# Kernel optimization log

Measured on AMD Instinct MI355X. Metric: run time of the kernel, lower is better.

## Reference

```python
import jax, jax.numpy as jnp
import numpy as np

DT = 0.05

def _conv(x, w):
    # x: [N,C,H,W], w: [O,I,kh,kw], SAME padding
    return jax.lax.conv_general_dilated(x, w, (1, 1), 'SAME',
                                        dimension_numbers=('NCHW', 'OIHW', 'NCHW'))

def _gru(h, x, wx, wh):
    # convolutional GRU cell (used for Bayesian jumps and SpatialGRU)
    xr, xz, xg = jnp.split(_conv(x, wx), 3, axis=1)
    hr, hz, hg = jnp.split(_conv(h, wh), 3, axis=1)
    r = jax.nn.sigmoid(xr + hr)
    z = jax.nn.sigmoid(xz + hz)
    g = jnp.tanh(xg + r * hg)
    return (1.0 - z) * h + z * g

def _ode_step(h, wrz, wg, dt):
    # GRU-ODE cell, explicit Euler: dh/dt = (1-z)*(g-h)
    r, z = jnp.split(jax.nn.sigmoid(_conv(h, wrz)), 2, axis=1)
    g = jnp.tanh(_conv(r * h, wg))
    return h + dt * (1.0 - z) * (g - h)

def _sgru(x, h0, wx, wh):
    # SpatialGRU: conv-GRU recurrence over the sequence dim
    def step(h, xt):
        h = _gru(h, xt, wx, wh)
        return h, h
    _, hs = jax.lax.scan(step, h0, x.transpose(1, 0, 2, 3, 4))
    return hs.transpose(1, 0, 2, 3, 4)

def setup_inputs() -> dict:
    key = jax.random.key(0)
    B, C, H, W = 2, 64, 64, 64
    Nc, Nl, NF = 3, 5, 6
    ks = jax.random.split(key, 16)
    f = lambda i, s: jax.random.normal(ks[i], s, jnp.float32)
    w = lambda i, s: 0.05 * jax.random.normal(ks[i], s, jnp.float32)
    inp = {}
    inp['future_prediction_input'] = f(0, (B, C, H, W))
    inp['camera_states'] = f(1, (B, Nc, C, H, W))
    inp['lidar_states'] = f(2, (B, Nl, C, H, W))
    # ragged obs times as exact multiples of DT; targets after all obs
    inp['camera_timestamp'] = jnp.broadcast_to(jnp.array([0., 2., 4.]) * DT, (B, Nc)).astype(jnp.float32)
    inp['lidar_timestamp'] = jnp.broadcast_to(jnp.array([1., 3., 5., 6., 7.]) * DT, (B, Nl)).astype(jnp.float32)
    inp['target_timestamp'] = jnp.broadcast_to(jnp.arange(8., 14.) * DT, (B, NF)).astype(jnp.float32)
    inp['ode_wrz'] = w(3, (2 * C, C, 3, 3))
    inp['ode_wg'] = w(4, (C, C, 3, 3))
    inp['jmp_wx'] = w(5, (3 * C, C, 3, 3))
    inp['jmp_wh'] = w(6, (3 * C, C, 3, 3))
    inp['sg0_wx'] = w(7, (3 * C, C, 3, 3))
    inp['sg0_wh'] = w(8, (3 * C, C, 3, 3))
    inp['sg1_wx'] = w(9, (3 * C, C, 3, 3))
    inp['sg1_wh'] = w(10, (3 * C, C, 3, 3))
    inp['res0_w1'] = w(11, (C, C, 3, 3))
    inp['res0_w2'] = w(12, (C, C, 3, 3))
    inp['dl_w1'] = w(13, (128, C, 3, 3))
    inp['dl_w2'] = w(14, (C, 128, 1, 1))
    return inp

def reference(future_prediction_input, camera_states, lidar_states,
              camera_timestamp, lidar_timestamp, target_timestamp,
              ode_wrz, ode_wg, jmp_wx, jmp_wh,
              sg0_wx, sg0_wh, sg1_wx, sg1_wh,
              res0_w1, res0_w2, dl_w1, dl_w2):
    dt = DT
    B, C, H, W = future_prediction_input.shape
    Nc, Nl, NF = camera_timestamp.shape[1], lidar_timestamp.shape[1], target_timestamp.shape[1]
    n_steps = Nc + Nl + NF  # static Euler grid covering all obs + target times
    # --- batched ragged merge: scatter obs onto the time grid (replaces per-sample dict sort) ---
    all_t = jnp.concatenate([camera_timestamp, lidar_timestamp], axis=1)          # [B, Nc+Nl]
    all_obs = jnp.concatenate([camera_states, lidar_states], axis=1)              # [B, Nc+Nl, C, H, W]
    steps = jnp.round(all_t / dt).astype(jnp.int32)
    bidx = jnp.arange(B)[:, None]
    grid = jnp.zeros((B, n_steps, C, H, W), all_obs.dtype).at[bidx, steps].set(all_obs)
    mask = jnp.zeros((B, n_steps), jnp.float32).at[bidx, steps].set(1.0)
    # --- ODE-RNN with Bayesian jumps: jump at obs, Euler-evolve between ---
    def ode_scan(h, xs):
        obs_t, m = xs
        hj = _gru(h, obs_t, jmp_wx, jmp_wh)
        h = jnp.where(m[:, None, None, None] > 0, hj, h)
        h = _ode_step(h, ode_wrz, ode_wg, dt)
        return h, h
    _, hs = jax.lax.scan(ode_scan, future_prediction_input,
                         (grid.transpose(1, 0, 2, 3, 4), mask.T))
    tsteps = jnp.round(target_timestamp / dt).astype(jnp.int32) - 1               # state after step k is time (k+1)*dt
    x = hs.transpose(1, 0, 2, 3, 4)[bidx, tsteps]                                 # [B, NF, C, H, W]
    auxilary_loss = jnp.float32(0.0)
    # --- spatial GRU stack + res blocks / DeepLab head ---
    hidden = x[:, 0]
    x = _sgru(x, hidden, sg0_wx, sg0_wh)
    xf = x.reshape(B * NF, C, H, W)
    xf = xf + _conv(jax.nn.relu(_conv(xf, res0_w1)), res0_w2)                     # residual Block
    x = xf.reshape(B, NF, C, H, W)
    x = _sgru(x, hidden, sg1_wx, sg1_wh)
    xf = x.reshape(B * NF, C, H, W)
    xf = _conv(jax.nn.relu(_conv(xf, dl_w1)), dl_w2)                              # DeepLabHead (3x3 -> relu -> 1x1)
    x = xf.reshape(B, NF, C, H, W)
    return (x, auxilary_loss)
```

## Files before the change

### kernel.cpp

```cpp
#include <hip/hip_runtime.h>
#include <stdint.h>

#define HWP 4096
#define SB  262144LL
#define FB  1572864LL
#define SLABU 1572864LL
#define DTC 0.05f

typedef short short4v __attribute__((ext_vector_type(4)));
typedef short short8v __attribute__((ext_vector_type(8)));
typedef float f32x16  __attribute__((ext_vector_type(16)));

__device__ __forceinline__ float sigm(float x) { return 1.f / (1.f + __expf(-x)); }
__device__ __forceinline__ float tanhf_(float x) {
  float a = fabsf(x);
  float t = __expf(-2.f * a);
  float r = (1.f - t) / (1.f + t);
  return x < 0.f ? -r : r;
}
__device__ __forceinline__ float gru1(float h, float xr, float hr, float xz,
                                      float hz, float xg, float hg) {
  float r = sigm(xr + hr);
  float z = sigm(xz + hz);
  float g = tanhf_(xg + r * hg);
  return (1.f - z) * h + z * g;
}
__device__ __forceinline__ float b2f(unsigned int u) {
  return __uint_as_float(u << 16);
}
__device__ __forceinline__ unsigned short f2b(float f) {
  unsigned int x = __float_as_uint(f);
  unsigned int r = (x + 0x7fffu + ((x >> 16) & 1u)) >> 16;
  return (unsigned short)r;
}

struct WJobs {
  const float* src[11];
  unsigned short* dst[11];
  int oc[11];
  int blk_off[12];
};

__global__ __launch_bounds__(256) void convert_all(WJobs jobs)
{
  int b = blockIdx.x;
  int j = 0;
  while (b >= jobs.blk_off[j + 1]) ++j;
  int g = (b - jobs.blk_off[j]) * 256 + threadIdx.x;
  if (g >= jobs.oc[j] * 64) return;
  const float* w = jobs.src[j];
  unsigned short* dst = jobs.dst[j];
  int oc = g >> 6, ic = g & 63;
  int ocg = oc >> 5, m = oc & 31;
  int kh = ic >> 4, ks = (ic >> 3) & 1, jj = ic & 7;
  int lane = m + 32 * ks;
#pragma unroll
  for (int t = 0; t < 9; ++t) {
    float v = w[(size_t)(oc * 64 + ic) * 9 + t];
    unsigned short hi = f2b(v);
    unsigned short lo = f2b(v - b2f(hi));
    size_t fb = ((size_t)(ocg * 4 + kh) * 9 + t) * 1024;
    dst[fb + (size_t)lane * 8 + jj] = hi;
    dst[fb + 512 + (size_t)lane * 8 + jj] = lo;
  }
}

__global__ __launch_bounds__(256) void convert_1x1(
    const float* __restrict__ w, unsigned short* __restrict__ dst)
{
  int g = blockIdx.x * 256 + threadIdx.x;
  if (g >= 64 * 128) return;
  int oc = g >> 7, ic = g & 127;
  int ocg = oc >> 5, m = oc & 31;
  int k = ic >> 4, ksub = (ic >> 3) & 1, j = ic & 7;
  int lane = m + 32 * ksub;
  float v = w[(size_t)oc * 128 + ic];
  unsigned short hi = f2b(v);
  unsigned short lo = f2b(v - b2f(hi));
  size_t fb = (size_t)(ocg * 8 + k) * 1024;
  dst[fb + (size_t)lane * 8 + j] = hi;
  dst[fb + 512 + (size_t)lane * 8 + j] = lo;
}

template<int NR>
__device__ __forceinline__ void stage_rows(
    unsigned short (*lds)[2][66][68], int slot0,
    const float* __restrict__ in_img, int gy0, int tid)
{
  int px = tid & 63, icq = tid >> 6;
  int ic0 = icq * 16;
  float v[NR][16];
#pragma unroll
  for (int r = 0; r < NR; ++r) {
    int gy = gy0 + r;
    if (gy >= 0 && gy < 64) {
#pragma unroll
      for (int i = 0; i < 16; ++i)
        v[r][i] = in_img[(size_t)(ic0 + i) * HWP + (size_t)gy * 64 + px];
    } else {
#pragma unroll
      for (int i = 0; i < 16; ++i) v[r][i] = 0.f;
    }
  }
#pragma unroll
  for (int r = 0; r < NR; ++r) {
    unsigned short hi[16], lo[16];
#pragma unroll
    for (int i = 0; i < 16; ++i) {
      hi[i] = f2b(v[r][i]);
      lo[i] = f2b(v[r][i] - b2f(hi[i]));
    }
    unsigned short* dhi = &lds[slot0 + r][0][px + 1][ic0];
    unsigned short* dlo = &lds[slot0 + r][1][px + 1][ic0];
#pragma unroll
    for (int q = 0; q < 4; ++q) {
      uint2 ph, pl;
      ph.x = (unsigned)hi[q*4+0] | ((unsigned)hi[q*4+1] << 16);
      ph.y = (unsigned)hi[q*4+2] | ((unsigned)hi[q*4+3] << 16);
      pl.x = (unsigned)lo[q*4+0] | ((unsigned)lo[q*4+1] << 16);
      pl.y = (unsigned)lo[q*4+2] | ((unsigned)lo[q*4+3] << 16);
      *(uint2*)&dhi[q*4] = ph;
      *(uint2*)&dlo[q*4] = pl;
    }
  }
}

#define LOAD_B_SLOT(SLOT, kx)                                                 \
  {                                                                           \
    const unsigned short* bph = &lds[SLOT][0][x0 + n + kx][khb];              \
    const unsigned short* bpl = &lds[SLOT][1][x0 + n + kx][khb];              \
    bhi.lo = *(const short4v*)bph; bhi.hi = *(const short4v*)(bph + 4);       \
    blo.lo = *(const short4v*)bpl; blo.hi = *(const short4v*)(bpl + 4);       \
  }

#define MFMA3(CACC, AHI, ALO)                                                 \
  CACC = __builtin_amdgcn_mfma_f32_32x32x16_bf16(AHI, bhi, CACC, 0, 0, 0);    \
  CACC = __builtin_amdgcn_mfma_f32_32x32x16_bf16(ALO, bhi, CACC, 0, 0, 0);    \
  CACC = __builtin_amdgcn_mfma_f32_32x32x16_bf16(AHI, blo, CACC, 0, 0, 0);

__global__ __launch_bounds__(256) void gru_mfma(
    const float* __restrict__ hprev, long long h_is,
    const unsigned short* __restrict__ wfrag,
    const unsigned short* __restrict__ xcs,
    float* __restrict__ hout, long long o_is)
{
  __shared__ __align__(16) unsigned short lds[3][2][66][68];
  int bid = blockIdx.x;
  int img = bid >> 6, y = bid & 63;
  int tid = threadIdx.x;
  int wv = tid >> 6, lane = tid & 63;
  int wchg = wv >> 1, wpx = wv & 1;
  int x0 = wpx * 32;
  int n = lane & 31, ksub = lane >> 5;

  const float* in_img = hprev + (size_t)img * h_is;
  for (int i = tid; i < 3366; i += 256)
    ((uint4*)lds)[i] = make_uint4(0u, 0u, 0u, 0u);
  __syncthreads();
  stage_rows<3>(lds, 0, in_img, y - 1, tid);
  __syncthreads();

  f32x16 cr, cz, cg;
#pragma unroll
  for (int i = 0; i < 16; ++i) { cr[i] = 0.f; cz[i] = 0.f; cg[i] = 0.f; }

#pragma unroll
  for (int kh = 0; kh < 4; ++kh) {
    int khb = kh * 16 + ksub * 8;
#pragma unroll
    for (int kidx = 0; kidx < 9; ++kidx) {
      int ky = kidx / 3, kx = kidx - ky * 3;
      short8v bhi, blo;
      LOAD_B_SLOT(ky, kx);
      const unsigned short* apr =
          wfrag + (((size_t)wchg * 4 + kh) * 9 + kidx) * 1024 + (size_t)lane * 8;
      const unsigned short* apz = apr + (size_t)2 * 4 * 9 * 1024;
      const unsigned short* apg = apr + (size_t)4 * 4 * 9 * 1024;
      short8v arh = *(const short8v*)apr;
      short8v arl = *(const short8v*)(apr + 512);
      short8v azh = *(const short8v*)apz;
      short8v azl = *(const short8v*)(apz + 512);
      short8v agh = *(const short8v*)apg;
      short8v agl = *(const short8v*)(apg + 512);
      MFMA3(cr, arh, arl);
      MFMA3(cz, azh, azl);
      MFMA3(cg, agh, agl);
    }
  }

  const unsigned short* xcb = xcs + (size_t)img * 786432;
#pragma unroll
  for (int reg = 0; reg < 16; ++reg) {
    int crow = (reg & 3) + 8 * (reg >> 2) + 4 * ksub;
    int c = wchg * 32 + crow;
    size_t px = (size_t)y * 64 + x0 + n;
    float xr = b2f(xcb[(size_t)c * HWP + px]);
    float xz = b2f(xcb[(size_t)(c + 64) * HWP + px]);
    float xg = b2f(xcb[(size_t)(c + 128) * HWP + px]);
    float hv = b2f(lds[1][0][x0 + n + 1][c]) + b2f(lds[1][1][x0 + n + 1][c]);
    hout[(size_t)img * o_is + (size_t)c * HWP + px] =
        gru1(hv, xr, cr[reg], xz, cz[reg], xg, cg[reg]);
  }
}

__global__ __launch_bounds__(256) void rzodeg_mfma(
    const float* __restrict__ hsrc,
    const unsigned short* __restrict__ wrzf,
    const unsigned short* __restrict__ wgf,
    float* __restrict__ hdst,
    float* __restrict__ fr, float* __restrict__ hid)
{
  __shared__ __align__(16) unsigned short lds[5][2][66][68];
  int bid = blockIdx.x;
  int img = bid >> 6, y = bid & 63;
  int tid = threadIdx.x;
  int wv = tid >> 6, lane = tid & 63;
  int wchg = wv >> 1, wpx = wv & 1;
  int x0 = wpx * 32;
  int n = lane & 31, ksub = lane >> 5;

  for (int i = tid; i < 5 * 4 * 16; i += 256) {
    int row = i >> 4, q = i & 15;
    int slot = row >> 2, rem = row & 3;
    int plane = rem >> 1;
    int col = (rem & 1) ? 65 : 0;
    ((uint2*)&lds[slot][plane][col][0])[q] = make_uint2(0u, 0u);
  }
  const float* in_img = hsrc + (size_t)img * SB;
  stage_rows<5>(lds, 0, in_img, y - 2, tid);
  __syncthreads();

  f32x16 cr0, cr1, cr2, cz;
#pragma unroll
  for (int i = 0; i < 16; ++i) { cr0[i]=0.f; cr1[i]=0.f; cr2[i]=0.f; cz[i]=0.f; }

#pragma unroll
  for (int kh = 0; kh < 4; ++kh) {
    int khb = kh * 16 + ksub * 8;
#pragma unroll
    for (int kidx = 0; kidx < 9; ++kidx) {
      int ky = kidx / 3, kx = kidx - ky * 3;
      const unsigned short* apr =
          wrzf + (((size_t)wchg * 4 + kh) * 9 + kidx) * 1024 + (size_t)lane * 8;
      const unsigned short* apz = apr + (size_t)2 * 4 * 9 * 1024;
      short8v arh = *(const short8v*)apr;
      short8v arl = *(const short8v*)(apr + 512);
      short8v azh = *(const short8v*)apz;
      short8v azl = *(const short8v*)(apz + 512);
      { short8v bhi, blo; LOAD_B_SLOT(ky, kx);     MFMA3(cr0, arh, arl); }
      { short8v bhi, blo; LOAD_B_SLOT(ky + 1, kx); MFMA3(cr1, arh, arl);
                                                   MFMA3(cz,  azh, azl); }
      { short8v bhi, blo; LOAD_B_SLOT(ky + 2, kx); MFMA3(cr2, arh, arl); }
    }
  }

  float rv0[16], rv1[16], rv2[16], hk[16];
  {
    int pc = x0 + n + 1;
#pragma unroll
    for (int reg = 0; reg < 16; ++reg) {
      int crow = (reg & 3) + 8 * (reg >> 2) + 4 * ksub;
      int c = wchg * 32 + crow;
      float h0 = b2f(lds[1][0][pc][c]) + b2f(lds[1][1][pc][c]);
      float h1 = b2f(lds[2][0][pc][c]) + b2f(lds[2][1][pc][c]);
      float h2 = b2f(lds[3][0][pc][c]) + b2f(lds[3][1][pc][c]);
      rv0[reg] = sigm(cr0[reg]) * h0;
      rv1[reg] = sigm(cr1[reg]) * h1;
      rv2[reg] = sigm(cr2[reg]) * h2;
      hk[reg] = h1;
    }
  }
  __syncthreads();

  {
    int pc = x0 + n + 1;
#pragma unroll
    for (int reg = 0; reg < 16; ++reg) {
      int crow = (reg & 3) + 8 * (reg >> 2) + 4 * ksub;
      int c = wchg * 32 + crow;
      unsigned short h0 = f2b(rv0[reg]), l0 = f2b(rv0[reg] - b2f(h0));
      unsigned short h1 = f2b(rv1[reg]), l1 = f2b(rv1[reg] - b2f(h1));
      unsigned short h2 = f2b(rv2[reg]), l2 = f2b(rv2[reg] - b2f(h2));
      lds[0][0][pc][c] = h0; lds[0][1][pc][c] = l0;
      lds[1][0][pc][c] = h1; lds[1][1][pc][c] = l1;
      lds[2][0][pc][c] = h2; lds[2][1][pc][c] = l2;
    }
  }
  __syncthreads();

  f32x16 cg;
#pragma unroll
  for (int i = 0; i < 16; ++i) cg[i] = 0.f;
#pragma unroll
  for (int kh = 0; kh < 4; ++kh) {
    int khb = kh * 16 + ksub * 8;
#pragma unroll
    for (int kidx = 0; kidx < 9; ++kidx) {
      int ky = kidx / 3, kx = kidx - ky * 3;
      const unsigned short* ap =
          wgf + (((size_t)wchg * 4 + kh) * 9 + kidx) * 1024 + (size_t)lane * 8;
      short8v ahi = *(const short8v*)ap;
      short8v alo = *(const short8v*)(ap + 512);
      short8v bhi, blo;
      LOAD_B_SLOT(ky, kx);
      MFMA3(cg, ahi, alo);
    }
  }

#pragma unroll
  for (int reg = 0; reg < 16; ++reg) {
    int crow = (reg & 3) + 8 * (reg >> 2) + 4 * ksub;
    int c = wchg * 32 + crow;
    size_t pxo = (size_t)y * 64 + x0 + n;
    size_t idx = (size_t)img * SB + (size_t)c * HWP + pxo;
    float z = sigm(cz[reg]);
    float h = hk[reg];
    float o = h + DTC * (1.f - z) * (tanhf_(cg[reg]) - h);
    hdst[idx] = o;
    if (fr)  fr[(size_t)img * FB + (size_t)c * HWP + pxo] = o;
    if (hid) hid[idx] = o;
  }
}

__global__ __launch_bounds__(256) void conv_mfma(
    const float* __restrict__ in_base, long long s1, long long s2,
    const float* __restrict__ cam, const float* __restrict__ lid, int s0,
    const unsigned short* __restrict__ wfrag, int OC,
    float* __restrict__ out_f32, unsigned short* __restrict__ out_b16,
    long long o1, long long o2, int flags)
{
  __shared__ __align__(16) unsigned short lds[4][2][66][68];

  int bpe = (OC >> 6) << 5;
  int bid = blockIdx.x;
  int e = bid / bpe; int r = bid - e * bpe;
  int ocb = r >> 5; int yb = r & 31;
  int y0 = yb << 1;
  int tid = threadIdx.x;
  int wv = tid >> 6, lane = tid & 63;
  int wocg = wv >> 1, wpx = wv & 1;
  int oc0w = ocb * 64 + wocg * 32;
  int x0 = wpx * 32;
  int n = lane & 31, ksub = lane >> 5;

  const float* in_img;
  if (cam) {
    int s = s0 + (e >> 1); int img = e & 1;
    int isLid = (0xEA >> s) & 1;
    int frm = isLid ? (s < 5 ? (s >> 1) : s - 3) : (s >> 1);
    in_img = isLid ? lid + ((size_t)img * 5 + frm) * SB
                   : cam + ((size_t)img * 3 + frm) * SB;
  } else {
    in_img = in_base + (size_t)(e >> 1) * s1 + (size_t)(e & 1) * s2;
  }
  size_t obase = (size_t)(e >> 1) * o1 + (size_t)(e & 1) * o2;

  for (int i = tid; i < 4488; i += 256)
    ((uint4*)lds)[i] = make_uint4(0u, 0u, 0u, 0u);
  __syncthreads();
  stage_rows<4>(lds, 0, in_img, y0 - 1, tid);
  __syncthreads();

  size_t wfbase = (size_t)(oc0w >> 5) * 4;

  f32x16 c0, c1;
#pragma unroll
  for (int i = 0; i < 16; ++i) { c0[i] = 0.f; c1[i] = 0.f; }

#pragma unroll
  for (int kh = 0; kh < 4; ++kh) {
    int khb = kh * 16 + ksub * 8;
#pragma unroll
    for (int kidx = 0; kidx < 9; ++kidx) {
      int ky = kidx / 3, kx = kidx - ky * 3;
      const unsigned short* ap =
          wfrag + ((wfbase + kh) * 9 + kidx) * 1024 + (size_t)lane * 8;
      short8v ahi = *(const short8v*)ap;
      short8v alo = *(const short8v*)(ap + 512);
      short8v bhi, blo;
      LOAD_B_SLOT(ky, kx);
      MFMA3(c0, ahi, alo);
      LOAD_B_SLOT(ky + 1, kx);
      MFMA3(c1, ahi, alo);
    }
  }

  auto epilogue = [&](const f32x16& c, int y) {
#pragma unroll
    for (int reg = 0; reg < 16; ++reg) {
      int row = (reg & 3) + 8 * (reg >> 2) + 4 * ksub;
      int oc = oc0w + row;
      float v = c[reg];
      if (flags & 1) v = fmaxf(v, 0.f);
      size_t off = obase + (size_t)oc * HWP + (size_t)y * 64 + (x0 + n);
      if (out_b16) {
        out_b16[off] = f2b(v);
      } else {
        if (flags & 2) v += out_f32[off];
        out_f32[off] = v;
      }
    }
  };
  epilogue(c0, y0);
  epilogue(c1, y0 + 1);
}

__global__ __launch_bounds__(256) void conv1x1_mfma(
    const unsigned short* __restrict__ in,
    const unsigned short* __restrict__ wfrag,
    float* __restrict__ out)
{
  __shared__ unsigned short lds1[64][132];
  int bid = blockIdx.x;
  int img = bid >> 6; int pt = bid & 63;
  int px0 = pt * 64;
  int tid = threadIdx.x;
  int wv = tid >> 6, lane = tid & 63;
  int wocg = wv >> 1, wpx = wv & 1;
  int x0 = wpx * 32;
  int n = lane & 31, ksub = lane >> 5;

  const unsigned short* ip = in + (size_t)img * 128 * HWP + px0;
  {
    int px = tid & 63, icq = tid >> 6;
#pragma unroll
    for (int i = 0; i < 32; ++i) {
      int ic = icq * 32 + i;
      lds1[px][ic] = ip[(size_t)ic * HWP + px];
    }
  }
  __syncthreads();

  f32x16 c;
#pragma unroll
  for (int i = 0; i < 16; ++i) c[i] = 0.f;

#pragma unroll
  for (int k = 0; k < 8; ++k) {
    const unsigned short* ap =
        wfrag + (size_t)(wocg * 8 + k) * 1024 + (size_t)lane * 8;
    short8v ahi = *(const short8v*)ap;
    short8v alo = *(const short8v*)(ap + 512);
    int khb = k * 16 + ksub * 8;
    const unsigned short* bp = &lds1[x0 + n][khb];
    short8v b;
    b.lo = *(const short4v*)bp; b.hi = *(const short4v*)(bp + 4);
    c = __builtin_amdgcn_mfma_f32_32x32x16_bf16(ahi, b, c, 0, 0, 0);
    c = __builtin_amdgcn_mfma_f32_32x32x16_bf16(alo, b, c, 0, 0, 0);
  }

#pragma unroll
  for (int reg = 0; reg < 16; ++reg) {
    int row = (reg & 3) + 8 * (reg >> 2) + 4 * ksub;
    int oc = wocg * 32 + row;
    out[((size_t)img * 64 + oc) * HWP + px0 + x0 + n] = c[reg];
  }
}

__global__ __launch_bounds__(256) void copy_k(
    const float* __restrict__ in, float* __restrict__ out)
{
  int i = blockIdx.x * 256 + threadIdx.x;
  ((float4*)out)[i] = ((const float4*)in)[i];
}

__global__ void aux_k(float* out) { out[0] = 0.f; }

extern "C" void kernel_launch(void* const* d_in, const int* in_sizes, int n_in,
                              void* d_out, int out_size, void* d_ws, size_t ws_size,
                              hipStream_t stream)
{
  const float* fpi = (const float*)d_in[0];
  const float* cam = (const float*)d_in[1];
  const float* lid = (const float*)d_in[2];
  const float* w_ode_rz = (const float*)d_in[6];
  const float* w_ode_g  = (const float*)d_in[7];
  const float* w_jmp_x  = (const float*)d_in[8];
  const float* w_jmp_h  = (const float*)d_in[9];
  const float* w_sg0_x  = (const float*)d_in[10];
  const float* w_sg0_h  = (const float*)d_in[11];
  const float* w_sg1_x  = (const float*)d_in[12];
  const float* w_sg1_h  = (const float*)d_in[13];
  const float* w_res_1  = (const float*)d_in[14];
  const float* w_res_2  = (const float*)d_in[15];
  const float* w_dl_1   = (const float*)d_in[16];
  const float* w_dl_2   = (const float*)d_in[17];

  float* ws     = (float*)d_ws;
  float* frames = ws;
  float* hidden = ws + 3145728;
  float* h_a    = ws + 3670016;
  float* h_b    = ws + 4194304;
  unsigned short* xcu  = (unsigned short*)(ws + 5505024);
  unsigned short* wbuf = (unsigned short*)(ws + 7864320);
  float* big_res = ws + 3670016;
  unsigned short* big_dl = (unsigned short*)(ws + 3670016);
  unsigned short* wdl2f  = (unsigned short*)(ws + 8785920);

  unsigned short* wjx  = wbuf;
  unsigned short* ws0x = wbuf + 221184;
  unsigned short* ws1x = wbuf + 442368;
  unsigned short* wre1 = wbuf + 663552;
  unsigned short* wre2 = wbuf + 737280;
  unsigned short* wdl1 = wbuf + 811008;
  unsigned short* wjh  = wbuf + 958464;
  unsigned short* ws0h = wbuf + 1179648;
  unsigned short* ws1h = wbuf + 1400832;
  unsigned short* wrz  = wbuf + 1622016;
  unsigned short* wg   = wbuf + 1769472;

  WJobs jobs;
  const float* srcs[11] = {w_jmp_x, w_sg0_x, w_sg1_x, w_jmp_h, w_sg0_h, w_sg1_h,
                           w_dl_1, w_ode_rz, w_res_1, w_res_2, w_ode_g};
  unsigned short* dsts[11] = {wjx, ws0x, ws1x, wjh, ws0h, ws1h,
                              wdl1, wrz, wre1, wre2, wg};
  int ocs[11] = {192, 192, 192, 192, 192, 192, 128, 128, 64, 64, 64};
  int off = 0;
  for (int j = 0; j < 11; ++j) {
    jobs.src[j] = srcs[j]; jobs.dst[j] = dsts[j]; jobs.oc[j] = ocs[j];
    jobs.blk_off[j] = off; off += ocs[j] / 4;
  }
  jobs.blk_off[11] = off;
  convert_all<<<off, 256, 0, stream>>>(jobs);
  convert_1x1<<<32, 256, 0, stream>>>(w_dl_2, wdl2f);

  copy_k<<<512, 256, 0, stream>>>(fpi, h_a);

  const int batch_s0[3] = {0, 3, 6};
  const int batch_t1[3] = {3, 6, 13};
  float* cur = h_a;
  for (int b = 0; b < 3; ++b) {
    int nobs = (b < 2) ? 3 : 2;
    conv_mfma<<<nobs * 2 * 3 * 32, 256, 0, stream>>>(
        nullptr, 0, 0, cam, lid, batch_s0[b], wjx, 192,
        nullptr, xcu, SLABU, 786432, 0);
    for (int t = batch_s0[b]; t < batch_t1[b]; ++t) {
      float* fr  = (t >= 7) ? frames + (long long)(t - 7) * SB : nullptr;
      float* hid = (t == 7) ? hidden : nullptr;
      if (t < 8) {
        gru_mfma<<<128, 256, 0, stream>>>(
            h_a, SB, wjh, xcu + (long long)(t - batch_s0[b]) * SLABU, h_b, SB);
        rzodeg_mfma<<<128, 256, 0, stream>>>(h_b, wrz, wg, h_a, fr, hid);
        cur = h_a;
      } else {
        float* dst = (cur == h_a) ? h_b : h_a;
        rzodeg_mfma<<<128, 256, 0, stream>>>(cur, wrz, wg, dst, fr, nullptr);
        cur = dst;
      }
    }
  }

  for (int b = 0; b < 2; ++b) {
    conv_mfma<<<576, 256, 0, stream>>>(frames + (long long)(b * 3) * SB, SB, FB,
                                       nullptr, nullptr, 0, ws0x, 192,
                                       nullptr, xcu, SLABU, 786432, 0);
    for (int tl = 0; tl < 3; ++tl) {
      int f = b * 3 + tl;
      const float* hp = (f == 0) ? hidden : frames + (long long)(f - 1) * SB;
      long long hbs = (f == 0) ? SB : FB;
      gru_mfma<<<128, 256, 0, stream>>>(hp, hbs, ws0h,
                                        xcu + (long long)tl * SLABU,
                                        frames + (long long)f * SB, FB);
    }
  }

  conv_mfma<<<384, 256, 0, stream>>>(frames, 2 * SB, SB, nullptr, nullptr, 0,
                                     wre1, 64, big_res, nullptr, 2 * SB, SB, 1);
  conv_mfma<<<384, 256, 0, stream>>>(big_res, 2 * SB, SB, nullptr, nullptr, 0,
                                     wre2, 64, frames, nullptr, 2 * SB, SB, 2);

  for (int b = 0; b < 2; ++b) {
    conv_mfma<<<576, 256, 0, stream>>>(frames + (long long)(b * 3) * SB, SB, FB,
                                       nullptr, nullptr, 0, ws1x, 192,
                                       nullptr, xcu, SLABU, 786432, 0);
    for (int tl = 0; tl < 3; ++tl) {
      int f = b * 3 + tl;
      const float* hp = (f == 0) ? hidden : frames + (long long)(f - 1) * SB;
      long long hbs = (f == 0) ? SB : FB;
      gru_mfma<<<128, 256, 0, stream>>>(hp, hbs, ws1h,
                                        xcu + (long long)tl * SLABU,
                                        frames + (long long)f * SB, FB);
    }
  }

  conv_mfma<<<768, 256, 0, stream>>>(frames, 2 * SB, SB, nullptr, nullptr, 0,
                                     wdl1, 128, nullptr, big_dl,
                                     1048576, 524288, 1);
  conv1x1_mfma<<<768, 256, 0, stream>>>(big_dl, wdl2f, (float*)d_out);

  aux_k<<<1, 1, 0, stream>>>((float*)d_out + 3145728);
}
```

Measured before the change: 1.090 ms.

## Overlap input-conv of future steps with recurrent GRU step in merged launches

Adds a combined kernel whose first 128 blocks run the recurrent GRU step and whose remaining blocks compute the input convolution for a later timestep, using a rotating ring of slabs. This replaces the batched input-conv launches and hides the low-occupancy 128-block GRU launches behind independent conv work, cutting launch count. It risks slab reuse hazards and gives the GRU blocks a larger LDS allocation, which may lower occupancy. The SpatialGRU stacks were also reorganized into one lambda using a four-slab buffer.

```diff
diff --git a/kernel.cpp b/kernel.cpp
--- a/kernel.cpp
+++ b/kernel.cpp
@@ -138,16 +138,14 @@
   CACC = __builtin_amdgcn_mfma_f32_32x32x16_bf16(ALO, bhi, CACC, 0, 0, 0);    \
   CACC = __builtin_amdgcn_mfma_f32_32x32x16_bf16(AHI, blo, CACC, 0, 0, 0);
 
-__global__ __launch_bounds__(256) void gru_mfma(
+__device__ void gru_body(
+    unsigned short (*lds)[2][66][68], int bid, int tid,
     const float* __restrict__ hprev, long long h_is,
     const unsigned short* __restrict__ wfrag,
     const unsigned short* __restrict__ xcs,
     float* __restrict__ hout, long long o_is)
 {
-  __shared__ __align__(16) unsigned short lds[3][2][66][68];
-  int bid = blockIdx.x;
   int img = bid >> 6, y = bid & 63;
-  int tid = threadIdx.x;
   int wv = tid >> 6, lane = tid & 63;
   int wchg = wv >> 1, wpx = wv & 1;
   int x0 = wpx * 32;
@@ -203,6 +201,128 @@
   }
 }
 
+__device__ void conv_body(
+    unsigned short (*lds)[2][66][68], int bid, int tid,
+    const float* __restrict__ in_base, long long s1, long long s2,
+    const float* __restrict__ cam, const float* __restrict__ lid, int s0,
+    const unsigned short* __restrict__ wfrag, int OC,
+    float* __restrict__ out_f32, unsigned short* __restrict__ out_b16,
+    long long o1, long long o2, int flags)
+{
+  int bpe = (OC >> 6) << 5;
+  int e = bid / bpe; int r = bid - e * bpe;
+  int ocb = r >> 5; int yb = r & 31;
+  int y0 = yb << 1;
+  int wv = tid >> 6, lane = tid & 63;
+  int wocg = wv >> 1, wpx = wv & 1;
+  int oc0w = ocb * 64 + wocg * 32;
+  int x0 = wpx * 32;
+  int n = lane & 31, ksub = lane >> 5;
+
+  const float* in_img;
+  if (cam) {
+    int s = s0 + (e >> 1); int img = e & 1;
+    int isLid = (0xEA >> s) & 1;
+    int frm = isLid ? (s < 5 ? (s >> 1) : s - 3) : (s >> 1);
+    in_img = isLid ? lid + ((size_t)img * 5 + frm) * SB
+                   : cam + ((size_t)img * 3 + frm) * SB;
+  } else {
+    in_img = in_base + (size_t)(e >> 1) * s1 + (size_t)(e & 1) * s2;
+  }
+  size_t obase = (size_t)(e >> 1) * o1 + (size_t)(e & 1) * o2;
+
+  for (int i = tid; i < 4488; i += 256)
+    ((uint4*)lds)[i] = make_uint4(0u, 0u, 0u, 0u);
+  __syncthreads();
+  stage_rows<4>(lds, 0, in_img, y0 - 1, tid);
+  __syncthreads();
+
+  size_t wfbase = (size_t)(oc0w >> 5) * 4;
+
+  f32x16 c0, c1;
+#pragma unroll
+  for (int i = 0; i < 16; ++i) { c0[i] = 0.f; c1[i] = 0.f; }
+
+#pragma unroll
+  for (int kh = 0; kh < 4; ++kh) {
+    int khb = kh * 16 + ksub * 8;
+#pragma unroll
+    for (int kidx = 0; kidx < 9; ++kidx) {
+      int ky = kidx / 3, kx = kidx - ky * 3;
+      const unsigned short* ap =
+          wfrag + ((wfbase + kh) * 9 + kidx) * 1024 + (size_t)lane * 8;
+      short8v ahi = *(const short8v*)ap;
+      short8v alo = *(const short8v*)(ap + 512);
+      short8v bhi, blo;
+      LOAD_B_SLOT(ky, kx);
+      MFMA3(c0, ahi, alo);
+      LOAD_B_SLOT(ky + 1, kx);
+      MFMA3(c1, ahi, alo);
+    }
+  }
+
+#pragma unroll
+  for (int iy = 0; iy < 2; ++iy) {
+    const f32x16& c = iy ? c1 : c0;
+    int y = y0 + iy;
+#pragma unroll
+    for (int reg = 0; reg < 16; ++reg) {
+      int row = (reg & 3) + 8 * (reg >> 2) + 4 * ksub;
+      int oc = oc0w + row;
+      float v = c[reg];
+      if (flags & 1) v = fmaxf(v, 0.f);
+      size_t off = obase + (size_t)oc * HWP + (size_t)y * 64 + (x0 + n);
+      if (out_b16) {
+        out_b16[off] = f2b(v);
+      } else {
+        if (flags & 2) v += out_f32[off];
+        out_f32[off] = v;
+      }
+    }
+  }
+}
+
+__global__ __launch_bounds__(256) void gru_mfma(
+    const float* __restrict__ hprev, long long h_is,
+    const unsigned short* __restrict__ wfrag,
+    const unsigned short* __restrict__ xcs,
+    float* __restrict__ hout, long long o_is)
+{
+  __shared__ __align__(16) unsigned short lds[3][2][66][68];
+  gru_body(lds, blockIdx.x, threadIdx.x, hprev, h_is, wfrag, xcs, hout, o_is);
+}
+
+__global__ __launch_bounds__(256) void conv_mfma(
+    const float* __restrict__ in_base, long long s1, long long s2,
+    const float* __restrict__ cam, const float* __restrict__ lid, int s0,
+    const unsigned short* __restrict__ wfrag, int OC,
+    float* __restrict__ out_f32, unsigned short* __restrict__ out_b16,
+    long long o1, long long o2, int flags)
+{
+  __shared__ __align__(16) unsigned short lds[4][2][66][68];
+  conv_body(lds, blockIdx.x, threadIdx.x, in_base, s1, s2, cam, lid, s0,
+            wfrag, OC, out_f32, out_b16, o1, o2, flags);
+}
+
+__global__ __launch_bounds__(256) void gru_conv_mfma(
+    const float* __restrict__ hprev, long long h_is,
+    const unsigned short* __restrict__ wfrag,
+    const unsigned short* __restrict__ xcs,
+    float* __restrict__ hout, long long o_is,
+    const float* __restrict__ cin, long long cs1, long long cs2,
+    const float* __restrict__ cam, const float* __restrict__ lid, int cs0,
+    const unsigned short* __restrict__ cwf,
+    unsigned short* __restrict__ cout, long long co2)
+{
+  __shared__ __align__(16) unsigned short lds[4][2][66][68];
+  if (blockIdx.x < 128) {
+    gru_body(lds, blockIdx.x, threadIdx.x, hprev, h_is, wfrag, xcs, hout, o_is);
+  } else {
+    conv_body(lds, blockIdx.x - 128, threadIdx.x, cin, cs1, cs2, cam, lid, cs0,
+              cwf, 192, nullptr, cout, SLABU, co2, 0);
+  }
+}
+
 __global__ __launch_bounds__(256) void rzodeg_mfma(
     const float* __restrict__ hsrc,
     const unsigned short* __restrict__ wrzf,
@@ -320,89 +440,6 @@
     if (fr)  fr[(size_t)img * FB + (size_t)c * HWP + pxo] = o;
     if (hid) hid[idx] = o;
   }
-}
-
-__global__ __launch_bounds__(256) void conv_mfma(
-    const float* __restrict__ in_base, long long s1, long long s2,
-    const float* __restrict__ cam, const float* __restrict__ lid, int s0,
-    const unsigned short* __restrict__ wfrag, int OC,
-    float* __restrict__ out_f32, unsigned short* __restrict__ out_b16,
-    long long o1, long long o2, int flags)
-{
-  __shared__ __align__(16) unsigned short lds[4][2][66][68];
-
-  int bpe = (OC >> 6) << 5;
-  int bid = blockIdx.x;
-  int e = bid / bpe; int r = bid - e * bpe;
-  int ocb = r >> 5; int yb = r & 31;
-  int y0 = yb << 1;
-  int tid = threadIdx.x;
-  int wv = tid >> 6, lane = tid & 63;
-  int wocg = wv >> 1, wpx = wv & 1;
-  int oc0w = ocb * 64 + wocg * 32;
-  int x0 = wpx * 32;
-  int n = lane & 31, ksub = lane >> 5;
-
-  const float* in_img;
-  if (cam) {
-    int s = s0 + (e >> 1); int img = e & 1;
-    int isLid = (0xEA >> s) & 1;
-    int frm = isLid ? (s < 5 ? (s >> 1) : s - 3) : (s >> 1);
-    in_img = isLid ? lid + ((size_t)img * 5 + frm) * SB
-                   : cam + ((size_t)img * 3 + frm) * SB;
-  } else {
-    in_img = in_base + (size_t)(e >> 1) * s1 + (size_t)(e & 1) * s2;
-  }
-  size_t obase = (size_t)(e >> 1) * o1 + (size_t)(e & 1) * o2;
-
-  for (int i = tid; i < 4488; i += 256)
-    ((uint4*)lds)[i] = make_uint4(0u, 0u, 0u, 0u);
-  __syncthreads();
-  stage_rows<4>(lds, 0, in_img, y0 - 1, tid);
-  __syncthreads();
-
-  size_t wfbase = (size_t)(oc0w >> 5) * 4;
-
-  f32x16 c0, c1;
-#pragma unroll
-  for (int i = 0; i < 16; ++i) { c0[i] = 0.f; c1[i] = 0.f; }
-
-#pragma unroll
-  for (int kh = 0; kh < 4; ++kh) {
-    int khb = kh * 16 + ksub * 8;
-#pragma unroll
-    for (int kidx = 0; kidx < 9; ++kidx) {
-      int ky = kidx / 3, kx = kidx - ky * 3;
-      const unsigned short* ap =
-          wfrag + ((wfbase + kh) * 9 + kidx) * 1024 + (size_t)lane * 8;
-      short8v ahi = *(const short8v*)ap;
-      short8v alo = *(const short8v*)(ap + 512);
-      short8v bhi, blo;
-      LOAD_B_SLOT(ky, kx);
-      MFMA3(c0, ahi, alo);
-      LOAD_B_SLOT(ky + 1, kx);
-      MFMA3(c1, ahi, alo);
-    }
-  }
-
-  auto epilogue = [&](const f32x16& c, int y) {
-#pragma unroll
-    for (int reg = 0; reg < 16; ++reg) {
-      int row = (reg & 3) + 8 * (reg >> 2) + 4 * ksub;
-      int oc = oc0w + row;
-      float v = c[reg];
-      if (flags & 1) v = fmaxf(v, 0.f);
-      size_t off = obase + (size_t)oc * HWP + (size_t)y * 64 + (x0 + n);
-      if (out_b16) {
-        out_b16[off] = f2b(v);
-      } else {
-        if (flags & 2) v += out_f32[off];
-        out_f32[off] = v;
-      }
-    }
-  };
-  epilogue(c0, y0);
-  epilogue(c1, y0 + 1);
 }
 
 __global__ __launch_bounds__(256) void conv1x1_mfma(
@@ -492,6 +529,7 @@
   float* h_a    = ws + 3670016;
   float* h_b    = ws + 4194304;
   unsigned short* xcu  = (unsigned short*)(ws + 5505024);
+  unsigned short* xcu4 = (unsigned short*)(ws + 4718592);
   unsigned short* wbuf = (unsigned short*)(ws + 7864320);
   float* big_res = ws + 3670016;
   unsigned short* big_dl = (unsigned short*)(ws + 3670016);
@@ -526,62 +564,60 @@
 
   copy_k<<<512, 256, 0, stream>>>(fpi, h_a);
 
-  const int batch_s0[3] = {0, 3, 6};
-  const int batch_t1[3] = {3, 6, 13};
+  conv_mfma<<<384, 256, 0, stream>>>(
+      nullptr, 0, 0, cam, lid, 0, wjx, 192, nullptr, xcu, SLABU, 786432, 0);
   float* cur = h_a;
-  for (int b = 0; b < 3; ++b) {
-    int nobs = (b < 2) ? 3 : 2;
-    conv_mfma<<<nobs * 2 * 3 * 32, 256, 0, stream>>>(
-        nullptr, 0, 0, cam, lid, batch_s0[b], wjx, 192,
-        nullptr, xcu, SLABU, 786432, 0);
-    for (int t = batch_s0[b]; t < batch_t1[b]; ++t) {
-      float* fr  = (t >= 7) ? frames + (long long)(t - 7) * SB : nullptr;
-      float* hid = (t == 7) ? hidden : nullptr;
-      if (t < 8) {
-        gru_mfma<<<128, 256, 0, stream>>>(
-            h_a, SB, wjh, xcu + (long long)(t - batch_s0[b]) * SLABU, h_b, SB);
-        rzodeg_mfma<<<128, 256, 0, stream>>>(h_b, wrz, wg, h_a, fr, hid);
-        cur = h_a;
+  for (int t = 0; t < 13; ++t) {
+    float* fr  = (t >= 7) ? frames + (long long)(t - 7) * SB : nullptr;
+    float* hid = (t == 7) ? hidden : nullptr;
+    if (t < 8) {
+      unsigned short* slab_r = xcu + (long long)(t % 3) * SLABU;
+      if (t < 6) {
+        int tc = t + 2;
+        gru_conv_mfma<<<320, 256, 0, stream>>>(
+            h_a, SB, wjh, slab_r, h_b, SB,
+            nullptr, 0, 0, cam, lid, tc, wjx,
+            xcu + (long long)(tc % 3) * SLABU, 786432);
       } else {
-        float* dst = (cur == h_a) ? h_b : h_a;
-        rzodeg_mfma<<<128, 256, 0, stream>>>(cur, wrz, wg, dst, fr, nullptr);
-        cur = dst;
+        gru_mfma<<<128, 256, 0, stream>>>(h_a, SB, wjh, slab_r, h_b, SB);
       }
-    }
-  }
-
-  for (int b = 0; b < 2; ++b) {
-    conv_mfma<<<576, 256, 0, stream>>>(frames + (long long)(b * 3) * SB, SB, FB,
-                                       nullptr, nullptr, 0, ws0x, 192,
-                                       nullptr, xcu, SLABU, 786432, 0);
-    for (int tl = 0; tl < 3; ++tl) {
-      int f = b * 3 + tl;
+      rzodeg_mfma<<<128, 256, 0, stream>>>(h_b, wrz, wg, h_a, fr, hid);
+      cur = h_a;
+    } else {
+      float* dst = (cur == h_a) ? h_b : h_a;
+      rzodeg_mfma<<<128, 256, 0, stream>>>(cur, wrz, wg, dst, fr, nullptr);
+      cur = dst;
+    }
+  }
+
+  auto sgru = [&](const unsigned short* wx, const unsigned short* wh) {
+    conv_mfma<<<576, 256, 0, stream>>>(frames, SB, FB, nullptr, nullptr, 0,
+                                       wx, 192, nullptr, xcu4, SLABU, 786432, 0);
+    for (int f = 0; f < 6; ++f) {
       const float* hp = (f == 0) ? hidden : frames + (long long)(f - 1) * SB;
       long long hbs = (f == 0) ? SB : FB;
-      gru_mfma<<<128, 256, 0, stream>>>(hp, hbs, ws0h,
-                                        xcu + (long long)tl * SLABU,
-                                        frames + (long long)f * SB, FB);
-    }
-  }
+      unsigned short* slab_r = xcu4 + (long long)(f % 4) * SLABU;
+      if (f < 3) {
+        int fc = f + 3;
+        gru_conv_mfma<<<320, 256, 0, stream>>>(
+            hp, hbs, wh, slab_r, frames + (long long)f * SB, FB,
+            frames + (long long)fc * SB, 0, FB, nullptr, nullptr, 0, wx,
+            xcu4 + (long long)(fc % 4) * SLABU, 786432);
+      } else {
+        gru_mfma<<<128, 256, 0, stream>>>(hp, hbs, wh, slab_r,
+                                          frames + (long long)f * SB, FB);
+      }
+    }
+  };
+
+  sgru(ws0x, ws0h);
 
   conv_mfma<<<384, 256, 0, stream>>>(frames, 2 * SB, SB, nullptr, nullptr, 0,
                                      wre1, 64, big_res, nullptr, 2 * SB, SB, 1);
   conv_mfma<<<384, 256, 0, stream>>>(big_res, 2 * SB, SB, nullptr, nullptr, 0,
                                      wre2, 64, frames, nullptr, 2 * SB, SB, 2);
 
-  for (int b = 0; b < 2; ++b) {
-    conv_mfma<<<576, 256, 0, stream>>>(frames + (long long)(b * 3) * SB, SB, FB,
-                                       nullptr, nullptr, 0, ws1x, 192,
-                                       nullptr, xcu, SLABU, 786432, 0);
-    for (int tl = 0; tl < 3; ++tl) {
-      int f = b * 3 + tl;
-      const float* hp = (f == 0) ? hidden : frames + (long long)(f - 1) * SB;
-      long long hbs = (f == 0) ? SB : FB;
-      gru_mfma<<<128, 256, 0, stream>>>(hp, hbs, ws1h,
-                                        xcu + (long long)tl * SLABU,
-                                        frames + (long long)f * SB, FB);
-    }
-  }
+  sgru(ws1x, ws1h);
 
   conv_mfma<<<768, 256, 0, stream>>>(frames, 2 * SB, SB, nullptr, nullptr, 0,
                                      wdl1, 128, nullptr, big_dl,
```

Result: slower. 1.174 ms (+7.8%).
